# Kernel tuning notes

Hardware: AMD Instinct MI355X
Metric: run time of the kernel (lower is better)

## Reference

```python
import jax, jax.numpy as jnp
import numpy as np

B, L, D, H = 4, 2048, 512, 8
HD = D // H  # 64
MAX_REL = 4


def setup_inputs() -> dict:
    key = jax.random.key(0)
    ks = jax.random.split(key, 13)
    s = 1.0 / np.sqrt(D)
    return {
        "q": jax.random.normal(ks[0], (B, L, D), jnp.float32),
        "k": jax.random.normal(ks[1], (B, L, D), jnp.float32),
        "v": jax.random.normal(ks[2], (B, L, D), jnp.float32),
        "Wq": jax.random.normal(ks[3], (D, D), jnp.float32) * s,
        "bq": jax.random.normal(ks[4], (D,), jnp.float32) * 0.01,
        "Wk": jax.random.normal(ks[5], (D, D), jnp.float32) * s,
        "bk": jax.random.normal(ks[6], (D,), jnp.float32) * 0.01,
        "Wv": jax.random.normal(ks[7], (D, D), jnp.float32) * s,
        "bv": jax.random.normal(ks[8], (D,), jnp.float32) * 0.01,
        "Wo": jax.random.normal(ks[9], (D, D), jnp.float32) * s,
        "bo": jax.random.normal(ks[10], (D,), jnp.float32) * 0.01,
        "rel_k_table": jax.random.normal(ks[11], (2 * MAX_REL + 1, HD), jnp.float32),
        "rel_v_table": jax.random.normal(ks[12], (2 * MAX_REL + 1, HD), jnp.float32),
    }


def _to_heads(x):
    # [B, L, D] -> [B, H, L, HD]
    b, l, d = x.shape
    return x.reshape(b, l, H, d // H).transpose(0, 2, 1, 3)


def reference(q, k, v, Wq, bq, Wk, bk, Wv, bv, Wo, bo, rel_k_table, rel_v_table):
    # NOTE: in the source, the relative-attention output is overwritten by the
    # plain SDPA call immediately after, so observable math = SDPA only.
    # rel_k_table / rel_v_table are dead parameters (zero gradient).
    relu = jax.nn.relu
    qh = _to_heads(relu(q @ Wq.T + bq))  # [B,H,L,HD]
    kh = _to_heads(relu(k @ Wk.T + bk))
    vh = _to_heads(relu(v @ Wv.T + bv))
    # scale by sqrt(d_key)=sqrt(512), matching the original (not sqrt(head_dim))
    scores = jnp.einsum("bhqd,bhkd->bhqk", qh, kh) / jnp.sqrt(jnp.float32(D))
    attn = jax.nn.softmax(scores, axis=-1)
    out = jnp.einsum("bhqk,bhkd->bhqd", attn, vh)  # [B,H,L,HD]
    out = out.transpose(0, 2, 1, 3).reshape(B, L, D)
    return relu(out @ Wo.T + bo)
```

## Files before the change

kernel.cpp:

```cpp
#include <hip/hip_runtime.h>
#include <hip/hip_bf16.h>

#define B_  4
#define L_  2048
#define D_  512
#define H_  8
#define HD_ 64
#define M_  (B_ * L_)

typedef __bf16 bf16;
typedef __attribute__((ext_vector_type(8)))  __bf16 bf16x8;
typedef __attribute__((ext_vector_type(4)))  __bf16 bf16x4;
typedef __attribute__((ext_vector_type(16))) float  f32x16;

__device__ __forceinline__ f32x16 mfma32(bf16x8 a, bf16x8 b, f32x16 c) {
    return __builtin_amdgcn_mfma_f32_32x32x16_bf16(a, b, c, 0, 0, 0);
}

__device__ __forceinline__ void pack_body(const float* __restrict__ src,
                                          bf16* __restrict__ dst, int R,
                                          int m0, int k0)
{
    __shared__ __align__(16) bf16 tile[64][76];
    const int t = threadIdx.x;
#pragma unroll
    for (int rep = 0; rep < 4; rep++) {
        const int idx = rep * 256 + t;
        const int r = idx >> 4, c4 = idx & 15;
        const float4 f = *(const float4*)(src + (size_t)(m0 + r) * 512 + k0 + c4 * 4);
        bf16x4 v; v[0] = (bf16)f.x; v[1] = (bf16)f.y; v[2] = (bf16)f.z; v[3] = (bf16)f.w;
        *(bf16x4*)(&tile[r][c4 * 4]) = v;
    }
    __syncthreads();
#pragma unroll
    for (int rep = 0; rep < 2; rep++) {
        const int s = rep * 256 + t;
        const int ml = s & 63, kpl = s >> 6;
        const bf16x4 lo = *(const bf16x4*)(&tile[ml][kpl * 8]);
        const bf16x4 hi4 = *(const bf16x4*)(&tile[ml][kpl * 8 + 4]);
        bf16x8 v;
#pragma unroll
        for (int e = 0; e < 4; e++) { v[e] = lo[e]; v[e + 4] = hi4[e]; }
        *(bf16x8*)(dst + ((size_t)(k0 / 8 + kpl) * R + m0 + ml) * 8) = v;
    }
}

__global__ __launch_bounds__(256) void pack_x(const float* __restrict__ src,
                                              bf16* __restrict__ dst, int R)
{
    pack_body(src, dst, R, blockIdx.x * 64, blockIdx.y * 64);
}

__global__ __launch_bounds__(256) void pack_w(const float* __restrict__ w0,
                                              const float* __restrict__ w1,
                                              const float* __restrict__ w2,
                                              const float* __restrict__ w3,
                                              bf16* __restrict__ dst)
{
    const float* src = blockIdx.z == 0 ? w0 : blockIdx.z == 1 ? w1
                     : blockIdx.z == 2 ? w2 : w3;
    bf16* d = dst + (size_t)blockIdx.z * 64 * 512 * 8;
    pack_body(src, d, 512, blockIdx.x * 64, blockIdx.y * 64);
}

template<int OUT_MODE>
__global__ __launch_bounds__(256, 2) void proj_kernel(
    const bf16* __restrict__ Xp, const bf16* __restrict__ Wp,
    const float* __restrict__ bias, void* __restrict__ outv, float postmul)
{
    const int w    = threadIdx.x >> 6;
    const int lane = threadIdx.x & 63;
    const int l31  = lane & 31;
    const int hi   = lane >> 5;
    const int m0 = blockIdx.x * 128;
    const int n0 = blockIdx.y * 64;
    const int mh = w & 1;
    const int nh = w >> 1;

    __shared__ __align__(16) bf16 Abuf[16][64][8];
    __shared__ __align__(16) bf16 Bbuf[8][64][8];

    f32x16 acc[2];
#pragma unroll
    for (int mi = 0; mi < 2; mi++)
#pragma unroll
        for (int r = 0; r < 16; r++) acc[mi][r] = 0.0f;

    auto ldA = [&](int f, int k0) -> bf16x8 {
        return *(const bf16x8*)(Xp + ((size_t)((k0 >> 3) + (f >> 2) * 2 + hi) * M_
                                      + m0 + (f & 3) * 32 + l31) * 8);
    };
    auto ldB = [&](int f, int k0) -> bf16x8 {
        return *(const bf16x8*)(Wp + ((size_t)((k0 >> 3) + (f >> 1) * 2 + hi) * 512
                                      + n0 + (f & 1) * 32 + l31) * 8);
    };

    bf16x8 ra[4], rb[2];
#pragma unroll
    for (int i = 0; i < 4; i++) ra[i] = ldA(w * 4 + i, 0);
#pragma unroll
    for (int i = 0; i < 2; i++) rb[i] = ldB(w * 2 + i, 0);

    for (int it = 0; it < 8; it++) {
        __syncthreads();
#pragma unroll
        for (int i = 0; i < 4; i++) *(bf16x8*)(&Abuf[w * 4 + i][lane][0]) = ra[i];
#pragma unroll
        for (int i = 0; i < 2; i++) *(bf16x8*)(&Bbuf[w * 2 + i][lane][0]) = rb[i];
        __syncthreads();
        const int kn = (it < 7 ? it + 1 : 7) * 64;
#pragma unroll
        for (int i = 0; i < 4; i++) ra[i] = ldA(w * 4 + i, kn);
#pragma unroll
        for (int i = 0; i < 2; i++) rb[i] = ldB(w * 2 + i, kn);
#pragma unroll
        for (int ks = 0; ks < 4; ks++) {
            const bf16x8 bfr = *(const bf16x8*)(&Bbuf[ks * 2 + nh][lane][0]);
#pragma unroll
            for (int mi = 0; mi < 2; mi++) {
                const bf16x8 afr = *(const bf16x8*)(&Abuf[ks * 4 + mh * 2 + mi][lane][0]);
                acc[mi] = mfma32(afr, bfr, acc[mi]);
            }
        }
    }

    const int col = n0 + nh * 32 + l31;
    const float bn = bias[col];
#pragma unroll
    for (int mi = 0; mi < 2; mi++)
#pragma unroll
        for (int r = 0; r < 16; r++) {
            const int row = m0 + (mh * 2 + mi) * 32 + (r & 3) + 8 * (r >> 2) + 4 * hi;
            float v = fmaxf(acc[mi][r] + bn, 0.0f);
            if (OUT_MODE == 2) {
                ((float*)outv)[(size_t)row * D_ + col] = v;
            } else {
                v *= postmul;
                const int b = row >> 11, l = row & (L_ - 1);
                const int h = col >> 6,  hd = col & (HD_ - 1);
                size_t idx;
                if (OUT_MODE == 0)
                    idx = ((size_t)(b * H_ + h) * L_ + l) * HD_ + hd;
                else
                    idx = (((size_t)(b * H_ + h) * 8 + (hd >> 3)) * L_ + l) * 8 + (hd & 7);
                ((bf16*)outv)[idx] = (bf16)v;
            }
        }
}

__global__ __launch_bounds__(256) void pack_v(
    const bf16* __restrict__ vh, bf16* __restrict__ Vp)
{
    __shared__ __align__(16) bf16 tile[64][72];
    const int bh = blockIdx.y, l0 = blockIdx.x * 64;
    const bf16* src = vh + (size_t)bh * L_ * HD_;
    bf16*       dst = Vp + (size_t)bh * 256 * 64 * 8;
    const int x = threadIdx.x;
#pragma unroll
    for (int m = 0; m < 2; m++) {
        const int s = m * 256 + x;
        const int l = s >> 3, c = s & 7;
        *(bf16x8*)(&tile[l][c * 8]) = *(const bf16x8*)(src + (size_t)(l0 + l) * HD_ + c * 8);
    }
    __syncthreads();
#pragma unroll
    for (int m = 0; m < 2; m++) {
        const int s = m * 256 + x;
        const int hd = s & 63, lc = s >> 6;
        bf16x8 v;
#pragma unroll
        for (int e = 0; e < 8; e++) {
            const int p = lc * 8 + e;
            const int t = p & 15;
            const int tp = (t & 3) | ((t & 4) << 1) | ((t & 8) >> 1);
            v[e] = tile[(p & 48) | tp][hd];
        }
        *(bf16x8*)(dst + ((size_t)(l0 / 8 + lc) * 64 + hd) * 8) = v;
    }
}

__global__ __launch_bounds__(256) void attn_kernel(
    const bf16* __restrict__ qh, const bf16* __restrict__ Kp,
    const bf16* __restrict__ Vp, bf16* __restrict__ Op)
{
    const int w    = threadIdx.x >> 6;
    const int lane = threadIdx.x & 63;
    const int l31  = lane & 31;
    const int hi   = lane >> 5;
    const int bh   = blockIdx.y;
    const int qb   = blockIdx.x * 128 + w * 32;

    const bf16* Q   = qh + (size_t)bh * L_ * HD_;
    const bf16* Kpb = Kp + (size_t)bh * 8 * L_ * 8;
    const bf16* Vpb = Vp + (size_t)bh * 256 * 64 * 8;

    __shared__ __align__(16) bf16 Kbuf[8][64][8];
    __shared__ __align__(16) bf16 Vbuf[8][64][8];
    __shared__ float Lw[4][32];

    bf16x8 qf[4];
#pragma unroll
    for (int ks = 0; ks < 4; ks++)
        qf[ks] = *(const bf16x8*)(Q + (size_t)(qb + l31) * HD_ + ks * 16 + hi * 8);

    f32x16 o[2];
#pragma unroll
    for (int hf = 0; hf < 2; hf++)
#pragma unroll
        for (int r = 0; r < 16; r++) o[hf][r] = 0.0f;
    float lsum = 0.0f;

    auto kga = [&](int f, int j0) {
        return Kpb + ((size_t)((f >> 1) * 2 + hi) * L_ + j0 + (f & 1) * 32 + l31) * 8;
    };
    auto vga = [&](int f, int j0) {
        return Vpb + ((size_t)(j0 / 8 + (f >> 1) * 2 + hi) * 64 + (f & 1) * 32 + l31) * 8;
    };

    bf16x8 kr[2], vr[2];
#pragma unroll
    for (int i = 0; i < 2; i++) {
        kr[i] = *(const bf16x8*)kga(w * 2 + i, 0);
        vr[i] = *(const bf16x8*)vga(w * 2 + i, 0);
    }

    for (int j0 = 0; j0 < L_; j0 += 64) {
        __syncthreads();
#pragma unroll
        for (int i = 0; i < 2; i++) {
            *(bf16x8*)(&Kbuf[w * 2 + i][lane][0]) = kr[i];
            *(bf16x8*)(&Vbuf[w * 2 + i][lane][0]) = vr[i];
        }
        __syncthreads();
        const int jn = (j0 + 64 < L_) ? j0 + 64 : j0;
#pragma unroll
        for (int i = 0; i < 2; i++) {
            kr[i] = *(const bf16x8*)kga(w * 2 + i, jn);
            vr[i] = *(const bf16x8*)vga(w * 2 + i, jn);
        }

        f32x16 s[2];
#pragma unroll
        for (int jt = 0; jt < 2; jt++)
#pragma unroll
            for (int r = 0; r < 16; r++) s[jt][r] = 0.0f;
#pragma unroll
        for (int ks = 0; ks < 4; ks++)
#pragma unroll
            for (int jt = 0; jt < 2; jt++) {
                const bf16x8 kfr = *(const bf16x8*)(&Kbuf[ks * 2 + jt][lane][0]);
                s[jt] = mfma32(kfr, qf[ks], s[jt]);
            }

#pragma unroll
        for (int jt = 0; jt < 2; jt++)
#pragma unroll
            for (int r = 0; r < 16; r++) {
                const float e = __builtin_amdgcn_exp2f(s[jt][r]);
                s[jt][r] = e;
                lsum += e;
            }

#pragma unroll
        for (int ksj = 0; ksj < 4; ksj++) {
            const f32x16& sv = s[ksj >> 1];
            const int b8 = (ksj & 1) * 8;
            bf16x8 pf;
#pragma unroll
            for (int u = 0; u < 8; u++) pf[u] = (bf16)sv[b8 + u];
#pragma unroll
            for (int hf = 0; hf < 2; hf++) {
                const bf16x8 vfr = *(const bf16x8*)(&Vbuf[ksj * 2 + hf][lane][0]);
                o[hf] = mfma32(pf, vfr, o[hf]);
            }
        }
    }

    lsum += __shfl_xor(lsum, 32);
    if (hi == 0) Lw[w][l31] = lsum;
    asm volatile("s_waitcnt lgkmcnt(0)" ::: "memory");

    const int b = bh >> 3, h = bh & 7;
#pragma unroll
    for (int r = 0; r < 16; r++) {
        const int rl = (r & 3) + 8 * (r >> 2) + 4 * hi;
        const float inv = 1.0f / Lw[w][rl];
        const int m = b * L_ + qb + rl;
#pragma unroll
        for (int hf = 0; hf < 2; hf++) {
            const int col = h * HD_ + hf * 32 + l31;
            Op[((size_t)(col >> 3) * M_ + m) * 8 + (col & 7)] = (bf16)(o[hf][r] * inv);
        }
    }
}

extern "C" void kernel_launch(void* const* d_in, const int* in_sizes, int n_in,
                              void* d_out, int out_size, void* d_ws, size_t ws_size,
                              hipStream_t stream)
{
    (void)in_sizes; (void)n_in; (void)out_size; (void)ws_size;
    const float* q  = (const float*)d_in[0];
    const float* k  = (const float*)d_in[1];
    const float* v  = (const float*)d_in[2];
    const float* Wq = (const float*)d_in[3];
    const float* bq = (const float*)d_in[4];
    const float* Wk = (const float*)d_in[5];
    const float* bk = (const float*)d_in[6];
    const float* Wv = (const float*)d_in[7];
    const float* bv = (const float*)d_in[8];
    const float* Wo = (const float*)d_in[9];
    const float* bo = (const float*)d_in[10];
    float* out = (float*)d_out;

    char* ws = (char*)d_ws;
    const size_t SZ = (size_t)8 * 1024 * 1024;
    bf16* P0 = (bf16*)(ws);
    bf16* qh = (bf16*)(ws + SZ);
    bf16* vh = (bf16*)(ws + 2 * SZ);
    bf16* Wp = (bf16*)(ws + 3 * SZ);
    bf16* Kp = (bf16*)(d_out);
    bf16* Vp = P0;
    bf16* Ob = vh;

    bf16* Wqp = Wp, *Wkp = Wp + (size_t)64 * 512 * 8, *Wvp = Wp + (size_t)2 * 64 * 512 * 8,
        * Wop = Wp + (size_t)3 * 64 * 512 * 8;

    const float SCALE_LOG2E = 0.06377946282349575f;

    dim3 pb(256);
    pack_w<<<dim3(8, 8, 4), pb, 0, stream>>>(Wq, Wk, Wv, Wo, Wp);

    dim3 pgrid(M_ / 128, D_ / 64);
    pack_x<<<dim3(M_ / 64, 8), pb, 0, stream>>>(q, P0, M_);
    proj_kernel<0><<<pgrid, pb, 0, stream>>>(P0, Wqp, bq, qh, SCALE_LOG2E);

    pack_x<<<dim3(M_ / 64, 8), pb, 0, stream>>>(k, P0, M_);
    proj_kernel<1><<<pgrid, pb, 0, stream>>>(P0, Wkp, bk, Kp, 1.0f);

    pack_x<<<dim3(M_ / 64, 8), pb, 0, stream>>>(v, P0, M_);
    proj_kernel<0><<<pgrid, pb, 0, stream>>>(P0, Wvp, bv, vh, 1.0f);

    pack_v<<<dim3(L_ / 64, B_ * H_), pb, 0, stream>>>(vh, Vp);

    attn_kernel<<<dim3(L_ / 128, B_ * H_), pb, 0, stream>>>(qh, Kp, Vp, Ob);

    proj_kernel<2><<<pgrid, pb, 0, stream>>>(Ob, Wop, bo, out, 1.0f);
}
```

Measured before the change: 215.6 us.

## Batch pack and projection launches, fuse V repack, double-buffer GEMM and attention

Merges the weight and q/k packing into one launch and runs the Q and K projections together in one grid. The V projection now writes the swizzled layout directly, so the pack_v kernel is gone. The projection and attention loops switch to double-buffered LDS with one barrier per iteration. Attention blocks shrink to 128 threads with 64 queries each, giving more blocks. This cuts launch count and intermediate traffic but adds runtime mode branching and more LDS per block.

Result: faster. 210.6 us (-2.4%).

```diff
diff --git a/kernel.cpp b/kernel.cpp
--- a/kernel.cpp
+++ b/kernel.cpp
@@ -45,29 +45,36 @@
     }
 }
 
+__global__ __launch_bounds__(256) void pack_all(
+    const float* __restrict__ q, const float* __restrict__ k,
+    const float* __restrict__ W0, const float* __restrict__ W1,
+    const float* __restrict__ W2, const float* __restrict__ W3,
+    bf16* __restrict__ Wp, bf16* __restrict__ P0, bf16* __restrict__ P1)
+{
+    const int z = blockIdx.z;
+    if (z < 4) {
+        if (blockIdx.x >= 8) return;
+        const float* src = z == 0 ? W0 : z == 1 ? W1 : z == 2 ? W2 : W3;
+        pack_body(src, Wp + (size_t)z * 64 * 512 * 8, 512, blockIdx.x * 64, blockIdx.y * 64);
+    } else {
+        pack_body(z == 4 ? q : k, z == 4 ? P0 : P1, M_, blockIdx.x * 64, blockIdx.y * 64);
+    }
+}
+
 __global__ __launch_bounds__(256) void pack_x(const float* __restrict__ src,
-                                              bf16* __restrict__ dst, int R)
-{
-    pack_body(src, dst, R, blockIdx.x * 64, blockIdx.y * 64);
-}
-
-__global__ __launch_bounds__(256) void pack_w(const float* __restrict__ w0,
-                                              const float* __restrict__ w1,
-                                              const float* __restrict__ w2,
-                                              const float* __restrict__ w3,
                                               bf16* __restrict__ dst)
 {
-    const float* src = blockIdx.z == 0 ? w0 : blockIdx.z == 1 ? w1
-                     : blockIdx.z == 2 ? w2 : w3;
-    bf16* d = dst + (size_t)blockIdx.z * 64 * 512 * 8;
-    pack_body(src, d, 512, blockIdx.x * 64, blockIdx.y * 64);
-}
-
-template<int OUT_MODE>
-__global__ __launch_bounds__(256, 2) void proj_kernel(
-    const bf16* __restrict__ Xp, const bf16* __restrict__ Wp,
-    const float* __restrict__ bias, void* __restrict__ outv, float postmul)
-{
+    pack_body(src, dst, M_, blockIdx.x * 64, blockIdx.y * 64);
+}
+
+struct PJob {
+    const bf16* X; const bf16* W; const float* bias; void* out;
+    float postmul; int mode;
+};
+
+__global__ __launch_bounds__(256) void proj_kernel(PJob j0, PJob j1)
+{
+    const PJob jb = (blockIdx.z == 0) ? j0 : j1;
     const int w    = threadIdx.x >> 6;
     const int lane = threadIdx.x & 63;
     const int l31  = lane & 31;
@@ -77,8 +84,8 @@
     const int mh = w & 1;
     const int nh = w >> 1;
 
-    __shared__ __align__(16) bf16 Abuf[16][64][8];
-    __shared__ __align__(16) bf16 Bbuf[8][64][8];
+    __shared__ __align__(16) bf16 Ab[2][16][64][8];
+    __shared__ __align__(16) bf16 Bb[2][8][64][8];
 
     f32x16 acc[2];
 #pragma unroll
@@ -87,12 +94,12 @@
         for (int r = 0; r < 16; r++) acc[mi][r] = 0.0f;
 
     auto ldA = [&](int f, int k0) -> bf16x8 {
-        return *(const bf16x8*)(Xp + ((size_t)((k0 >> 3) + (f >> 2) * 2 + hi) * M_
-                                      + m0 + (f & 3) * 32 + l31) * 8);
+        return *(const bf16x8*)(jb.X + ((size_t)((k0 >> 3) + (f >> 2) * 2 + hi) * M_
+                                        + m0 + (f & 3) * 32 + l31) * 8);
     };
     auto ldB = [&](int f, int k0) -> bf16x8 {
-        return *(const bf16x8*)(Wp + ((size_t)((k0 >> 3) + (f >> 1) * 2 + hi) * 512
-                                      + n0 + (f & 1) * 32 + l31) * 8);
+        return *(const bf16x8*)(jb.W + ((size_t)((k0 >> 3) + (f >> 1) * 2 + hi) * 512
+                                        + n0 + (f & 1) * 32 + l31) * 8);
     };
 
     bf16x8 ra[4], rb[2];
@@ -100,86 +107,70 @@
     for (int i = 0; i < 4; i++) ra[i] = ldA(w * 4 + i, 0);
 #pragma unroll
     for (int i = 0; i < 2; i++) rb[i] = ldB(w * 2 + i, 0);
+#pragma unroll
+    for (int i = 0; i < 4; i++) *(bf16x8*)(&Ab[0][w * 4 + i][lane][0]) = ra[i];
+#pragma unroll
+    for (int i = 0; i < 2; i++) *(bf16x8*)(&Bb[0][w * 2 + i][lane][0]) = rb[i];
+    __syncthreads();
 
     for (int it = 0; it < 8; it++) {
-        __syncthreads();
-#pragma unroll
-        for (int i = 0; i < 4; i++) *(bf16x8*)(&Abuf[w * 4 + i][lane][0]) = ra[i];
-#pragma unroll
-        for (int i = 0; i < 2; i++) *(bf16x8*)(&Bbuf[w * 2 + i][lane][0]) = rb[i];
-        __syncthreads();
-        const int kn = (it < 7 ? it + 1 : 7) * 64;
-#pragma unroll
-        for (int i = 0; i < 4; i++) ra[i] = ldA(w * 4 + i, kn);
-#pragma unroll
-        for (int i = 0; i < 2; i++) rb[i] = ldB(w * 2 + i, kn);
+        const int cur = it & 1;
+        if (it < 7) {
+            const int kn = (it + 1) * 64;
+#pragma unroll
+            for (int i = 0; i < 4; i++) ra[i] = ldA(w * 4 + i, kn);
+#pragma unroll
+            for (int i = 0; i < 2; i++) rb[i] = ldB(w * 2 + i, kn);
+        }
 #pragma unroll
         for (int ks = 0; ks < 4; ks++) {
-            const bf16x8 bfr = *(const bf16x8*)(&Bbuf[ks * 2 + nh][lane][0]);
+            const bf16x8 bfr = *(const bf16x8*)(&Bb[cur][ks * 2 + nh][lane][0]);
 #pragma unroll
             for (int mi = 0; mi < 2; mi++) {
-                const bf16x8 afr = *(const bf16x8*)(&Abuf[ks * 4 + mh * 2 + mi][lane][0]);
+                const bf16x8 afr = *(const bf16x8*)(&Ab[cur][ks * 4 + mh * 2 + mi][lane][0]);
                 acc[mi] = mfma32(afr, bfr, acc[mi]);
             }
         }
+        if (it < 7) {
+#pragma unroll
+            for (int i = 0; i < 4; i++) *(bf16x8*)(&Ab[1 - cur][w * 4 + i][lane][0]) = ra[i];
+#pragma unroll
+            for (int i = 0; i < 2; i++) *(bf16x8*)(&Bb[1 - cur][w * 2 + i][lane][0]) = rb[i];
+            __syncthreads();
+        }
     }
 
     const int col = n0 + nh * 32 + l31;
-    const float bn = bias[col];
+    const float bn = jb.bias[col];
+    const int mode = jb.mode;
 #pragma unroll
     for (int mi = 0; mi < 2; mi++)
 #pragma unroll
         for (int r = 0; r < 16; r++) {
             const int row = m0 + (mh * 2 + mi) * 32 + (r & 3) + 8 * (r >> 2) + 4 * hi;
             float v = fmaxf(acc[mi][r] + bn, 0.0f);
-            if (OUT_MODE == 2) {
-                ((float*)outv)[(size_t)row * D_ + col] = v;
+            if (mode == 2) {
+                ((float*)jb.out)[(size_t)row * D_ + col] = v;
             } else {
-                v *= postmul;
+                v *= jb.postmul;
                 const int b = row >> 11, l = row & (L_ - 1);
                 const int h = col >> 6,  hd = col & (HD_ - 1);
+                const int bh = b * H_ + h;
                 size_t idx;
-                if (OUT_MODE == 0)
-                    idx = ((size_t)(b * H_ + h) * L_ + l) * HD_ + hd;
-                else
-                    idx = (((size_t)(b * H_ + h) * 8 + (hd >> 3)) * L_ + l) * 8 + (hd & 7);
-                ((bf16*)outv)[idx] = (bf16)v;
+                if (mode == 0) {
+                    idx = ((size_t)bh * L_ + l) * HD_ + hd;
+                } else if (mode == 1) {
+                    idx = (((size_t)bh * 8 + (hd >> 3)) * L_ + l) * 8 + (hd & 7);
+                } else {
+                    const int swzl = (l & ~15) | (l & 3) | ((l & 4) << 1) | ((l & 8) >> 1);
+                    idx = (((size_t)bh * 256 + (swzl >> 3)) * 64 + hd) * 8 + (swzl & 7);
+                }
+                ((bf16*)jb.out)[idx] = (bf16)v;
             }
         }
 }
 
-__global__ __launch_bounds__(256) void pack_v(
-    const bf16* __restrict__ vh, bf16* __restrict__ Vp)
-{
-    __shared__ __align__(16) bf16 tile[64][72];
-    const int bh = blockIdx.y, l0 = blockIdx.x * 64;
-    const bf16* src = vh + (size_t)bh * L_ * HD_;
-    bf16*       dst = Vp + (size_t)bh * 256 * 64 * 8;
-    const int x = threadIdx.x;
-#pragma unroll
-    for (int m = 0; m < 2; m++) {
-        const int s = m * 256 + x;
-        const int l = s >> 3, c = s & 7;
-        *(bf16x8*)(&tile[l][c * 8]) = *(const bf16x8*)(src + (size_t)(l0 + l) * HD_ + c * 8);
-    }
-    __syncthreads();
-#pragma unroll
-    for (int m = 0; m < 2; m++) {
-        const int s = m * 256 + x;
-        const int hd = s & 63, lc = s >> 6;
-        bf16x8 v;
-#pragma unroll
-        for (int e = 0; e < 8; e++) {
-            const int p = lc * 8 + e;
-            const int t = p & 15;
-            const int tp = (t & 3) | ((t & 4) << 1) | ((t & 8) >> 1);
-            v[e] = tile[(p & 48) | tp][hd];
-        }
-        *(bf16x8*)(dst + ((size_t)(l0 / 8 + lc) * 64 + hd) * 8) = v;
-    }
-}
-
-__global__ __launch_bounds__(256) void attn_kernel(
+__global__ __launch_bounds__(128) void attn_kernel(
     const bf16* __restrict__ qh, const bf16* __restrict__ Kp,
     const bf16* __restrict__ Vp, bf16* __restrict__ Op)
 {
@@ -188,91 +179,103 @@
     const int l31  = lane & 31;
     const int hi   = lane >> 5;
     const int bh   = blockIdx.y;
-    const int qb   = blockIdx.x * 128 + w * 32;
+    const int qb   = blockIdx.x * 64 + w * 32;
 
     const bf16* Q   = qh + (size_t)bh * L_ * HD_;
     const bf16* Kpb = Kp + (size_t)bh * 8 * L_ * 8;
     const bf16* Vpb = Vp + (size_t)bh * 256 * 64 * 8;
 
-    __shared__ __align__(16) bf16 Kbuf[8][64][8];
-    __shared__ __align__(16) bf16 Vbuf[8][64][8];
-    __shared__ float Lw[4][32];
+    __shared__ __align__(16) bf16 Kb[2][8][64][8];
+    __shared__ __align__(16) bf16 Vb[2][8][64][8];
+    __shared__ float Lw[2][32];
 
     bf16x8 qf[4];
 #pragma unroll
     for (int ks = 0; ks < 4; ks++)
         qf[ks] = *(const bf16x8*)(Q + (size_t)(qb + l31) * HD_ + ks * 16 + hi * 8);
 
-    f32x16 o[2];
-#pragma unroll
-    for (int hf = 0; hf < 2; hf++)
-#pragma unroll
-        for (int r = 0; r < 16; r++) o[hf][r] = 0.0f;
+    f32x16 zz;
+#pragma unroll
+    for (int r = 0; r < 16; r++) zz[r] = 0.0f;
+    f32x16 o0 = zz, o1 = zz;
     float lsum = 0.0f;
 
-    auto kga = [&](int f, int j0) {
-        return Kpb + ((size_t)((f >> 1) * 2 + hi) * L_ + j0 + (f & 1) * 32 + l31) * 8;
-    };
-    auto vga = [&](int f, int j0) {
-        return Vpb + ((size_t)(j0 / 8 + (f >> 1) * 2 + hi) * 64 + (f & 1) * 32 + l31) * 8;
-    };
-
-    bf16x8 kr[2], vr[2];
-#pragma unroll
-    for (int i = 0; i < 2; i++) {
-        kr[i] = *(const bf16x8*)kga(w * 2 + i, 0);
-        vr[i] = *(const bf16x8*)vga(w * 2 + i, 0);
-    }
-
-    for (int j0 = 0; j0 < L_; j0 += 64) {
-        __syncthreads();
-#pragma unroll
-        for (int i = 0; i < 2; i++) {
-            *(bf16x8*)(&Kbuf[w * 2 + i][lane][0]) = kr[i];
-            *(bf16x8*)(&Vbuf[w * 2 + i][lane][0]) = vr[i];
-        }
-        __syncthreads();
-        const int jn = (j0 + 64 < L_) ? j0 + 64 : j0;
-#pragma unroll
-        for (int i = 0; i < 2; i++) {
-            kr[i] = *(const bf16x8*)kga(w * 2 + i, jn);
-            vr[i] = *(const bf16x8*)vga(w * 2 + i, jn);
-        }
-
-        f32x16 s[2];
-#pragma unroll
-        for (int jt = 0; jt < 2; jt++)
-#pragma unroll
-            for (int r = 0; r < 16; r++) s[jt][r] = 0.0f;
-#pragma unroll
-        for (int ks = 0; ks < 4; ks++)
-#pragma unroll
-            for (int jt = 0; jt < 2; jt++) {
-                const bf16x8 kfr = *(const bf16x8*)(&Kbuf[ks * 2 + jt][lane][0]);
-                s[jt] = mfma32(kfr, qf[ks], s[jt]);
+    const bf16* kp[4];
+    const bf16* vp[4];
+#pragma unroll
+    for (int i = 0; i < 4; i++) {
+        const int f = w * 4 + i;
+        kp[i] = Kpb + ((size_t)((f >> 1) * 2 + hi) * L_ + (f & 1) * 32 + l31) * 8;
+        vp[i] = Vpb + ((size_t)((f >> 1) * 2 + hi) * 64 + (f & 1) * 32 + l31) * 8;
+    }
+
+    bf16x8 kr[4], vr[4];
+#pragma unroll
+    for (int i = 0; i < 4; i++) {
+        kr[i] = *(const bf16x8*)kp[i]; kp[i] += 512;
+        vr[i] = *(const bf16x8*)vp[i]; vp[i] += 4096;
+    }
+#pragma unroll
+    for (int i = 0; i < 4; i++) {
+        *(bf16x8*)(&Kb[0][w * 4 + i][lane][0]) = kr[i];
+        *(bf16x8*)(&Vb[0][w * 4 + i][lane][0]) = vr[i];
+    }
+    __syncthreads();
+
+    for (int t = 0; t < 32; t++) {
+        const int cur = t & 1;
+        if (t < 31) {
+#pragma unroll
+            for (int i = 0; i < 4; i++) {
+                kr[i] = *(const bf16x8*)kp[i]; kp[i] += 512;
+                vr[i] = *(const bf16x8*)vp[i]; vp[i] += 4096;
             }
-
-#pragma unroll
-        for (int jt = 0; jt < 2; jt++)
-#pragma unroll
-            for (int r = 0; r < 16; r++) {
-                const float e = __builtin_amdgcn_exp2f(s[jt][r]);
-                s[jt][r] = e;
-                lsum += e;
+        }
+
+        f32x16 s0 = mfma32(*(const bf16x8*)(&Kb[cur][0][lane][0]), qf[0], zz);
+        f32x16 s1 = mfma32(*(const bf16x8*)(&Kb[cur][1][lane][0]), qf[0], zz);
+#pragma unroll
+        for (int ks = 1; ks < 4; ks++) {
+            s0 = mfma32(*(const bf16x8*)(&Kb[cur][ks * 2 + 0][lane][0]), qf[ks], s0);
+            s1 = mfma32(*(const bf16x8*)(&Kb[cur][ks * 2 + 1][lane][0]), qf[ks], s1);
+        }
+
+#pragma unroll
+        for (int r = 0; r < 16; r++) {
+            const float e = __builtin_amdgcn_exp2f(s0[r]);
+            s0[r] = e; lsum += e;
+        }
+        {
+            bf16x8 pf0, pf1;
+#pragma unroll
+            for (int u = 0; u < 8; u++) { pf0[u] = (bf16)s0[u]; pf1[u] = (bf16)s0[8 + u]; }
+            o0 = mfma32(pf0, *(const bf16x8*)(&Vb[cur][0][lane][0]), o0);
+            o1 = mfma32(pf0, *(const bf16x8*)(&Vb[cur][1][lane][0]), o1);
+            o0 = mfma32(pf1, *(const bf16x8*)(&Vb[cur][2][lane][0]), o0);
+            o1 = mfma32(pf1, *(const bf16x8*)(&Vb[cur][3][lane][0]), o1);
+        }
+#pragma unroll
+        for (int r = 0; r < 16; r++) {
+            const float e = __builtin_amdgcn_exp2f(s1[r]);
+            s1[r] = e; lsum += e;
+        }
+        {
+            bf16x8 pf2, pf3;
+#pragma unroll
+            for (int u = 0; u < 8; u++) { pf2[u] = (bf16)s1[u]; pf3[u] = (bf16)s1[8 + u]; }
+            o0 = mfma32(pf2, *(const bf16x8*)(&Vb[cur][4][lane][0]), o0);
+            o1 = mfma32(pf2, *(const bf16x8*)(&Vb[cur][5][lane][0]), o1);
+            o0 = mfma32(pf3, *(const bf16x8*)(&Vb[cur][6][lane][0]), o0);
+            o1 = mfma32(pf3, *(const bf16x8*)(&Vb[cur][7][lane][0]), o1);
+        }
+
+        if (t < 31) {
+#pragma unroll
+            for (int i = 0; i < 4; i++) {
+                *(bf16x8*)(&Kb[1 - cur][w * 4 + i][lane][0]) = kr[i];
+                *(bf16x8*)(&Vb[1 - cur][w * 4 + i][lane][0]) = vr[i];
             }
-
-#pragma unroll
-        for (int ksj = 0; ksj < 4; ksj++) {
-            const f32x16& sv = s[ksj >> 1];
-            const int b8 = (ksj & 1) * 8;
-            bf16x8 pf;
-#pragma unroll
-            for (int u = 0; u < 8; u++) pf[u] = (bf16)sv[b8 + u];
-#pragma unroll
-            for (int hf = 0; hf < 2; hf++) {
-                const bf16x8 vfr = *(const bf16x8*)(&Vbuf[ksj * 2 + hf][lane][0]);
-                o[hf] = mfma32(pf, vfr, o[hf]);
-            }
+            __syncthreads();
         }
     }
 
@@ -286,10 +289,13 @@
         const int rl = (r & 3) + 8 * (r >> 2) + 4 * hi;
         const float inv = 1.0f / Lw[w][rl];
         const int m = b * L_ + qb + rl;
-#pragma unroll
-        for (int hf = 0; hf < 2; hf++) {
-            const int col = h * HD_ + hf * 32 + l31;
-            Op[((size_t)(col >> 3) * M_ + m) * 8 + (col & 7)] = (bf16)(o[hf][r] * inv);
+        {
+            const int col = h * HD_ + l31;
+            Op[((size_t)(col >> 3) * M_ + m) * 8 + (col & 7)] = (bf16)(o0[r] * inv);
+        }
+        {
+            const int col = h * HD_ + 32 + l31;
+            Op[((size_t)(col >> 3) * M_ + m) * 8 + (col & 7)] = (bf16)(o1[r] * inv);
         }
     }
 }
@@ -313,36 +319,36 @@
     float* out = (float*)d_out;
 
     char* ws = (char*)d_ws;
-    const size_t SZ = (size_t)8 * 1024 * 1024;
-    bf16* P0 = (bf16*)(ws);
-    bf16* qh = (bf16*)(ws + SZ);
-    bf16* vh = (bf16*)(ws + 2 * SZ);
-    bf16* Wp = (bf16*)(ws + 3 * SZ);
-    bf16* Kp = (bf16*)(d_out);
-    bf16* Vp = P0;
-    bf16* Ob = vh;
-
-    bf16* Wqp = Wp, *Wkp = Wp + (size_t)64 * 512 * 8, *Wvp = Wp + (size_t)2 * 64 * 512 * 8,
-        * Wop = Wp + (size_t)3 * 64 * 512 * 8;
+    const size_t MB = 1024 * 1024;
+    bf16* P0  = (bf16*)(ws);
+    bf16* P1  = (bf16*)(ws + 8 * MB);
+    bf16* Wp  = (bf16*)(ws + 16 * MB);
+    bf16* Vp  = (bf16*)(ws + 18 * MB);
+    bf16* qh  = (bf16*)(d_out);
+    bf16* Kp  = (bf16*)((char*)d_out + 8 * MB);
+    bf16* Opb = P0;
+
+    bf16* Wqp = Wp;
+    bf16* Wkp = Wp + (size_t)64 * 512 * 8;
+    bf16* Wvp = Wp + (size_t)2 * 64 * 512 * 8;
+    bf16* Wop = Wp + (size_t)3 * 64 * 512 * 8;
 
     const float SCALE_LOG2E = 0.06377946282349575f;
 
     dim3 pb(256);
-    pack_w<<<dim3(8, 8, 4), pb, 0, stream>>>(Wq, Wk, Wv, Wo, Wp);
-
-    dim3 pgrid(M_ / 128, D_ / 64);
-    pack_x<<<dim3(M_ / 64, 8), pb, 0, stream>>>(q, P0, M_);
-    proj_kernel<0><<<pgrid, pb, 0, stream>>>(P0, Wqp, bq, qh, SCALE_LOG2E);
-
-    pack_x<<<dim3(M_ / 64, 8), pb, 0, stream>>>(k, P0, M_);
-    proj_kernel<1><<<pgrid, pb, 0, stream>>>(P0, Wkp, bk, Kp, 1.0f);
-
-    pack_x<<<dim3(M_ / 64, 8), pb, 0, stream>>>(v, P0, M_);
-    proj_kernel<0><<<pgrid, pb, 0, stream>>>(P0, Wvp, bv, vh, 1.0f);
-
-    pack_v<<<dim3(L_ / 64, B_ * H_), pb, 0, stream>>>(vh, Vp);
-
-    attn_kernel<<<dim3(L_ / 128, B_ * H_), pb, 0, stream>>>(qh, Kp, Vp, Ob);
-
-    proj_kernel<2><<<pgrid, pb, 0, stream>>>(Ob, Wop, bo, out, 1.0f);
-}
+    pack_all<<<dim3(128, 8, 6), pb, 0, stream>>>(q, k, Wq, Wk, Wv, Wo, Wp, P0, P1);
+
+    PJob jq{P0, Wqp, bq, qh, SCALE_LOG2E, 0};
+    PJob jk{P1, Wkp, bk, Kp, 1.0f, 1};
+    proj_kernel<<<dim3(64, 8, 2), pb, 0, stream>>>(jq, jk);
+
+    pack_x<<<dim3(128, 8), pb, 0, stream>>>(v, P1);
+
+    PJob jv{P1, Wvp, bv, Vp, 1.0f, 3};
+    proj_kernel<<<dim3(64, 8, 1), pb, 0, stream>>>(jv, jv);
+
+    attn_kernel<<<dim3(L_ / 64, B_ * H_), dim3(128), 0, stream>>>(qh, Kp, Vp, Opb);
+
+    PJob jo{Opb, Wop, bo, out, 1.0f, 2};
+    proj_kernel<<<dim3(64, 8, 1), pb, 0, stream>>>(jo, jo);
+}
```
